# Kernel optimization log

Measured on AMD Instinct MI355X. Metric: run time of the kernel, lower is better.

The kernel has to match this reference:

```python
import jax, jax.numpy as jnp
import numpy as np
import math

D_MODEL = 1024
NHEAD = 16
D_HEAD = D_MODEL // NHEAD
TAU = 300.0
DELTA = 5.0 * 60.0  # delta_minutes -> seconds


def setup_inputs() -> dict:
    key = jax.random.key(0)
    ks = jax.random.split(key, 10)
    B, M = 4, 2048
    H = jax.random.normal(ks[0], (B, M, D_MODEL), dtype=jnp.float32)
    patch_mask = jax.random.randint(ks[1], (B, M), 0, 2).astype(jnp.int32)
    s = 1.0 / math.sqrt(D_MODEL)
    Wq = jax.random.normal(ks[2], (D_MODEL, D_MODEL), dtype=jnp.float32) * s
    bq = jnp.zeros((D_MODEL,), dtype=jnp.float32)
    Wk = jax.random.normal(ks[3], (D_MODEL, D_MODEL), dtype=jnp.float32) * s
    bk = jnp.zeros((D_MODEL,), dtype=jnp.float32)
    Wv = jax.random.normal(ks[4], (D_MODEL, D_MODEL), dtype=jnp.float32) * s
    bv = jnp.zeros((D_MODEL,), dtype=jnp.float32)
    Wo = jax.random.normal(ks[5], (D_MODEL, D_MODEL), dtype=jnp.float32) * s
    bo = jnp.zeros((D_MODEL,), dtype=jnp.float32)
    return {"H": H, "patch_mask": patch_mask, "Wq": Wq, "bq": bq,
            "Wk": Wk, "bk": bk, "Wv": Wv, "bv": bv, "Wo": Wo, "bo": bo}


def _time_bias(M):
    idx = jnp.arange(M)
    dist = jnp.abs(idx[:, None] - idx[None, :]).astype(jnp.float32) * DELTA
    w = jnp.exp(-dist / max(TAU, 1e-6))
    return jnp.log(w + 1e-12)  # (M, M)


def reference(H, patch_mask, Wq, bq, Wk, bk, Wv, bv, Wo, bo):
    B, M, D = H.shape
    nh, dh = NHEAD, D_HEAD
    # projections -> (B, nh, M, dh)
    q = (H @ Wq.T + bq).reshape(B, M, nh, dh).transpose(0, 2, 1, 3)
    k = (H @ Wk.T + bk).reshape(B, M, nh, dh).transpose(0, 2, 1, 3)
    v = (H @ Wv.T + bv).reshape(B, M, nh, dh).transpose(0, 2, 1, 3)
    attn = jnp.einsum('bhqd,bhkd->bhqk', q, k) / math.sqrt(dh)
    attn = attn + _time_bias(M)[None, None, :, :]
    key_pad = patch_mask <= 0  # (B, M)
    attn = jnp.where(key_pad[:, None, None, :], -1e9, attn)
    A = jax.nn.softmax(attn, axis=-1)
    out = jnp.einsum('bhqk,bhkd->bhqd', A, v)
    out = out.transpose(0, 2, 1, 3).reshape(B, M, D)
    out = out @ Wo.T + bo
    out = out * patch_mask[:, :, None].astype(out.dtype)
    return out
```

## Files before the change

### kernel.cpp

```cpp
#include <hip/hip_runtime.h>
#include <stdint.h>

typedef short short8 __attribute__((ext_vector_type(8)));
typedef float f32x4 __attribute__((ext_vector_type(4)));

#define B_    4
#define M_    2048
#define D_    1024
#define NH_   16
#define DH_   64
#define LOG2E 1.44269504f

__device__ __forceinline__ short f2bf(float f) {
  union { float f; uint32_t u; } v; v.f = f;
  uint32_t r = (v.u + 0x7fffu + ((v.u >> 16) & 1u)) >> 16;
  return (short)r;
}

__device__ __forceinline__ void gl_lds16(const void* g, void* l) {
  __builtin_amdgcn_global_load_lds(
      (__attribute__((address_space(1))) void*)(g),
      (__attribute__((address_space(3))) void*)(l),
      16, 0, 0);
}

__device__ __forceinline__ f32x4 mfma16(short8 a, short8 b, f32x4 c) {
  return __builtin_amdgcn_mfma_f32_16x16x32_bf16(a, b, c, 0, 0, 0);
}

__global__ __launch_bounds__(256) void cvt_all(const float* __restrict__ H,
                                               const float* __restrict__ s0,
                                               const float* __restrict__ s1,
                                               const float* __restrict__ s2,
                                               const float* __restrict__ s3,
                                               short* __restrict__ dH,
                                               short* __restrict__ d0,
                                               short* __restrict__ d1,
                                               short* __restrict__ d2,
                                               short* __restrict__ d3) {
  const int bidx = blockIdx.x;
  const float* src;
  short* dst;
  int i;
  if (bidx < 8192) {
    src = H; dst = dH; i = bidx * 256 + threadIdx.x;
  } else {
    const int y = (bidx - 8192) >> 10;
    src = (y == 0) ? s0 : (y == 1) ? s1 : (y == 2) ? s2 : s3;
    dst = (y == 0) ? d0 : (y == 1) ? d1 : (y == 2) ? d2 : d3;
    i = ((bidx - 8192) & 1023) * 256 + threadIdx.x;
  }
  float4 v = ((const float4*)src)[i];
  short4 o;
  o.x = f2bf(v.x); o.y = f2bf(v.y); o.z = f2bf(v.z); o.w = f2bf(v.w);
  ((short4*)dst)[i] = o;
}

__global__ __launch_bounds__(256, 3) void gemm_qkv(const short* __restrict__ A,
                                                   const short* __restrict__ Wqb,
                                                   const short* __restrict__ Wkb,
                                                   const short* __restrict__ Wvb,
                                                   const float* __restrict__ bq,
                                                   const float* __restrict__ bk,
                                                   const float* __restrict__ bv,
                                                   short* __restrict__ Qo,
                                                   short* __restrict__ Ko,
                                                   short* __restrict__ Vo) {
  __shared__ char smem_raw[34816];
  short* Ab0 = (short*)smem_raw;
  short* Ab1 = (short*)(smem_raw + 8192);
  short* Bb0 = (short*)(smem_raw + 16384);
  short* Bb1 = (short*)(smem_raw + 24576);

  const int L = blockIdx.x + 8 * (blockIdx.y + 64 * blockIdx.z);
  const int xcd = L & 7;
  const int s = L >> 3;
  const int m_local = s & 7;
  const int nz = s >> 3;
  const int nt = nz & 7, z = nz >> 3;
  const int m0 = (xcd * 8 + m_local) * 128;
  const int n0 = nt * 128;

  const short* Bt = (z == 0) ? Wqb : (z == 1) ? Wkb : Wvb;
  const float* bias = (z == 0) ? bq : (z == 1) ? bk : bv;
  const float scale = (z == 0) ? 0.125f : 1.0f;

  const int tid = threadIdx.x;
  const int w = tid >> 6, l = tid & 63;
  const int q4 = l >> 4, c = l & 15;
  const int wr = w >> 1, wc = w & 1;

  f32x4 acc[4][4] = {};
  const int arow = (l >> 2);
  const int acol = (l & 3) * 8;

#pragma unroll
  for (int st = 0; st < 2; ++st) {
    const int chunk = w * 2 + st;
    gl_lds16(A + (size_t)(m0 + chunk * 16 + arow) * 1024 + acol, Ab0 + chunk * 512);
    gl_lds16(Bt + (size_t)(n0 + chunk * 16 + arow) * 1024 + acol, Bb0 + chunk * 512);
  }
  __syncthreads();

  for (int kk = 0; kk < 32; ++kk) {
    const int cur = kk & 1;
    if (kk + 1 < 32) {
      const int k0n = (kk + 1) * 32;
#pragma unroll
      for (int st = 0; st < 2; ++st) {
        const int chunk = w * 2 + st;
        gl_lds16(A + (size_t)(m0 + chunk * 16 + arow) * 1024 + k0n + acol,
                 (cur ? Ab0 : Ab1) + chunk * 512);
        gl_lds16(Bt + (size_t)(n0 + chunk * 16 + arow) * 1024 + k0n + acol,
                 (cur ? Bb0 : Bb1) + chunk * 512);
      }
    }
    const short* Ab = cur ? Ab1 : Ab0;
    const short* Bb = cur ? Bb1 : Bb0;
    short8 af[4], bfr[4];
#pragma unroll
    for (int i = 0; i < 4; ++i)
      af[i] = *(const short8*)(Ab + (wr * 64 + i * 16 + c) * 32 + q4 * 8);
#pragma unroll
    for (int j = 0; j < 4; ++j)
      bfr[j] = *(const short8*)(Bb + (wc * 64 + j * 16 + c) * 32 + q4 * 8);
#pragma unroll
    for (int i = 0; i < 4; ++i)
#pragma unroll
      for (int j = 0; j < 4; ++j)
        acc[i][j] = mfma16(af[i], bfr[j], acc[i][j]);
    __syncthreads();
  }

  if (z < 2) {
    short* Cb = (short*)smem_raw;
    short* out = (z == 0) ? Qo : Ko;
#pragma unroll
    for (int j = 0; j < 4; ++j) {
      const float bvv = bias[n0 + wc * 64 + j * 16 + c];
#pragma unroll
      for (int i = 0; i < 4; ++i)
#pragma unroll
        for (int r = 0; r < 4; ++r)
          Cb[(wr * 64 + i * 16 + q4 * 4 + r) * 136 + wc * 64 + j * 16 + c] =
              f2bf((acc[i][j][r] + bvv) * scale);
    }
    __syncthreads();
#pragma unroll
    for (int p = 0; p < 8; ++p) {
      const int g = p * 256 + tid;
      const int row = g >> 4, seg = g & 15;
      *(short8*)(out + (size_t)(m0 + row) * 1024 + n0 + seg * 8) =
          *(const short8*)(Cb + row * 136 + seg * 8);
    }
  } else {
    short* Cb = (short*)smem_raw;
#pragma unroll
    for (int j = 0; j < 4; ++j) {
      const float bvv = bias[n0 + wc * 64 + j * 16 + c];
#pragma unroll
      for (int i = 0; i < 4; ++i) {
        short4 pk;
        pk.x = f2bf(acc[i][j][0] + bvv);
        pk.y = f2bf(acc[i][j][1] + bvv);
        pk.z = f2bf(acc[i][j][2] + bvv);
        pk.w = f2bf(acc[i][j][3] + bvv);
        *(short4*)(Cb + (wc * 64 + j * 16 + c) * 136 + wr * 64 + i * 16 + q4 * 4) = pk;
      }
    }
    __syncthreads();
    const int bb = m0 >> 11;
    const int tokb = m0 & 2047;
#pragma unroll
    for (int p = 0; p < 8; ++p) {
      const int g = p * 256 + tid;
      const int col = g >> 4, rseg = g & 15;
      const int colg = n0 + col;
      const int hh = colg >> 6, dd = colg & 63;
      *(short8*)(Vo + ((size_t)(bb * NH_ + hh) * DH_ + dd) * M_ + tokb + rseg * 8) =
          *(const short8*)(Cb + col * 136 + rseg * 8);
    }
  }
}

__global__ __launch_bounds__(256) void gemm_oproj(const short* __restrict__ A,
                                                  const short* __restrict__ Bt,
                                                  const float* __restrict__ bias,
                                                  const int* __restrict__ pmask,
                                                  float* __restrict__ outp) {
  __shared__ char smem[24576];
  short* Ab0 = (short*)smem;
  short* Ab1 = (short*)(smem + 8192);
  short* Bb0 = (short*)(smem + 16384);
  short* Bb1 = (short*)(smem + 20480);

  const int L = blockIdx.x + 16 * blockIdx.y;
  const int xcd = L & 7;
  const int s = L >> 3;
  const int m_local = s & 7;
  const int nt = s >> 3;
  const int m0 = (xcd * 8 + m_local) * 128;
  const int n0 = nt * 64;

  const int tid = threadIdx.x;
  const int w = tid >> 6, l = tid & 63;
  const int q4 = l >> 4, c = l & 15;
  const int wr = w >> 1, wc = w & 1;

  f32x4 acc[4][2] = {};
  const int arow = (l >> 2);
  const int acol = (l & 3) * 8;

#pragma unroll
  for (int st = 0; st < 2; ++st) {
    const int chunk = w * 2 + st;
    gl_lds16(A + (size_t)(m0 + chunk * 16 + arow) * 1024 + acol, Ab0 + chunk * 512);
  }
  gl_lds16(Bt + (size_t)(n0 + w * 16 + arow) * 1024 + acol, Bb0 + w * 512);
  __syncthreads();

  for (int kk = 0; kk < 32; ++kk) {
    const int cur = kk & 1;
    if (kk + 1 < 32) {
      const int k0n = (kk + 1) * 32;
#pragma unroll
      for (int st = 0; st < 2; ++st) {
        const int chunk = w * 2 + st;
        gl_lds16(A + (size_t)(m0 + chunk * 16 + arow) * 1024 + k0n + acol,
                 (cur ? Ab0 : Ab1) + chunk * 512);
      }
      gl_lds16(Bt + (size_t)(n0 + w * 16 + arow) * 1024 + k0n + acol,
               (cur ? Bb0 : Bb1) + w * 512);
    }
    const short* Ab = cur ? Ab1 : Ab0;
    const short* Bb = cur ? Bb1 : Bb0;
    short8 af[4], bfr[2];
#pragma unroll
    for (int i = 0; i < 4; ++i)
      af[i] = *(const short8*)(Ab + (wr * 64 + i * 16 + c) * 32 + q4 * 8);
#pragma unroll
    for (int j = 0; j < 2; ++j)
      bfr[j] = *(const short8*)(Bb + (wc * 32 + j * 16 + c) * 32 + q4 * 8);
#pragma unroll
    for (int i = 0; i < 4; ++i)
#pragma unroll
      for (int j = 0; j < 2; ++j)
        acc[i][j] = mfma16(af[i], bfr[j], acc[i][j]);
    __syncthreads();
  }

  float* Cf = (float*)smem;
#pragma unroll
  for (int half = 0; half < 2; ++half) {
    __syncthreads();
    if (wr == half) {
#pragma unroll
      for (int j = 0; j < 2; ++j) {
        const float bvv = bias[n0 + wc * 32 + j * 16 + c];
#pragma unroll
        for (int i = 0; i < 4; ++i)
#pragma unroll
          for (int r = 0; r < 4; ++r)
            Cf[(i * 16 + q4 * 4 + r) * 68 + wc * 32 + j * 16 + c] =
                acc[i][j][r] + bvv;
      }
    }
    __syncthreads();
#pragma unroll
    for (int p = 0; p < 4; ++p) {
      const int g = p * 256 + tid;
      const int row = g >> 4, seg = g & 15;
      const int rowg = m0 + half * 64 + row;
      const float mmv = (pmask[rowg] > 0) ? 1.0f : 0.0f;
      float4 v = *(const float4*)(Cf + row * 68 + seg * 4);
      v.x *= mmv; v.y *= mmv; v.z *= mmv; v.w *= mmv;
      *(float4*)(outp + (size_t)rowg * 1024 + n0 + seg * 4) = v;
    }
  }
}

__global__ __launch_bounds__(256) void attn_kernel(const short* __restrict__ Qb,
                                                   const short* __restrict__ Kb,
                                                   const short* __restrict__ Vtb,
                                                   const int* __restrict__ pmask,
                                                   short* __restrict__ Attb) {
  __shared__ char smem[20480];
  short* Ks0 = (short*)smem;
  short* Ks1 = (short*)(smem + 4096);
  short* Vs0 = (short*)(smem + 8192);
  short* Vs1 = (short*)(smem + 12288);
  short* Ps  = (short*)(smem + 16384);

  const int tid = threadIdx.x;
  const int w = tid >> 6, l = tid & 63;
  const int q4 = l >> 4, c = l & 15;
  const int qt = blockIdx.x, h = blockIdx.y, b = blockIdx.z;
  const short* Qrow = Qb + (size_t)(b * M_) * D_ + h * DH_;
  const short* Kbase = Kb + (size_t)(b * M_) * D_ + h * DH_;
  const short* Vbase = Vtb + (size_t)(b * NH_ + h) * DH_ * M_;
  const int qrow0 = qt * 64 + w * 16;

  short8 aq0 = *(const short8*)(Qrow + (size_t)(qrow0 + c) * D_ + q4 * 8);
  short8 aq1 = *(const short8*)(Qrow + (size_t)(qrow0 + c) * D_ + 32 + q4 * 8);

  const int jt0 = max(0, 2 * qt - 2);
  const int jt1 = min(M_ / 32 - 1, 2 * qt + 3);

  const int kh = tid >> 7, krow = (tid >> 2) & 31, ch = tid & 3;
  const int vrow = tid >> 2;

  {
    const int j0 = jt0 * 32;
    gl_lds16(Kbase + (size_t)(j0 + krow) * D_ + kh * 32 + ch * 8, (char*)Ks0 + tid * 16);
    gl_lds16(Vbase + (size_t)vrow * M_ + j0 + ch * 8, (char*)Vs0 + tid * 16);
  }
  __syncthreads();

  f32x4 o[4] = {};
  float lrun[4] = {0.f, 0.f, 0.f, 0.f};
  short* Pw = Ps + w * 512;

  for (int jt = jt0; jt <= jt1; ++jt) {
    const int buf = (jt - jt0) & 1;
    const int j0 = jt * 32;
    if (jt < jt1) {
      const int j0n = j0 + 32;
      gl_lds16(Kbase + (size_t)(j0n + krow) * D_ + kh * 32 + ch * 8,
               (char*)(buf ? Ks0 : Ks1) + tid * 16);
      gl_lds16(Vbase + (size_t)vrow * M_ + j0n + ch * 8,
               (char*)(buf ? Vs0 : Vs1) + tid * 16);
    }
    const short* Kt = buf ? Ks1 : Ks0;
    const short* Vt = buf ? Vs1 : Vs0;
    short8 b00 = *(const short8*)(Kt + c * 32 + q4 * 8);
    short8 b10 = *(const short8*)(Kt + 1024 + c * 32 + q4 * 8);
    short8 b01 = *(const short8*)(Kt + (16 + c) * 32 + q4 * 8);
    short8 b11 = *(const short8*)(Kt + 1024 + (16 + c) * 32 + q4 * 8);
    f32x4 s0 = {}, s1 = {};
    s0 = mfma16(aq0, b00, s0);
    s0 = mfma16(aq1, b10, s0);
    s1 = mfma16(aq0, b01, s1);
    s1 = mfma16(aq1, b11, s1);

    const float w0m = (pmask[b * M_ + j0 + c] > 0) ? 1.f : 0.f;
    const float w1m = (pmask[b * M_ + j0 + 16 + c] > 0) ? 1.f : 0.f;

#pragma unroll
    for (int r = 0; r < 4; ++r) {
      const int qr = qrow0 + q4 * 4 + r;
      const float d0 = fminf(fabsf((float)(qr - (j0 + c))), 28.0f);
      const float d1 = fminf(fabsf((float)(qr - (j0 + 16 + c))), 28.0f);
      const float p0 = exp2f((s0[r] - d0) * LOG2E) * w0m;
      const float p1 = exp2f((s1[r] - d1) * LOG2E) * w1m;
      Pw[(q4 * 4 + r) * 32 + c] = f2bf(p0);
      Pw[(q4 * 4 + r) * 32 + 16 + c] = f2bf(p1);
      lrun[r] += p0 + p1;
    }
    short8 pa = *(const short8*)(Pw + c * 32 + q4 * 8);
#pragma unroll
    for (int f = 0; f < 4; ++f) {
      short8 bv = *(const short8*)(Vt + (f * 16 + c) * 32 + q4 * 8);
      o[f] = mfma16(pa, bv, o[f]);
    }
    __syncthreads();
  }

#pragma unroll
  for (int r = 0; r < 4; ++r) {
#pragma unroll
    for (int off = 1; off < 16; off <<= 1)
      lrun[r] += __shfl_xor(lrun[r], off);
  }

  short* Cb = (short*)smem;
#pragma unroll
  for (int r = 0; r < 4; ++r) {
    const float inv = 1.0f / lrun[r];
#pragma unroll
    for (int f = 0; f < 4; ++f)
      Cb[(w * 16 + q4 * 4 + r) * 72 + f * 16 + c] = f2bf(o[f][r] * inv);
  }
  __syncthreads();
#pragma unroll
  for (int p = 0; p < 2; ++p) {
    const int u = p * 256 + tid;
    const int row = u >> 3, seg = u & 7;
    *(short8*)(Attb + (size_t)(b * M_ + qt * 64 + row) * D_ + h * DH_ + seg * 8) =
        *(const short8*)(Cb + row * 72 + seg * 8);
  }
}

extern "C" void kernel_launch(void* const* d_in, const int* in_sizes, int n_in,
                              void* d_out, int out_size, void* d_ws, size_t ws_size,
                              hipStream_t stream) {
  const float* H     = (const float*)d_in[0];
  const int*   pmask = (const int*)d_in[1];
  const float* Wq    = (const float*)d_in[2];
  const float* bq    = (const float*)d_in[3];
  const float* Wk    = (const float*)d_in[4];
  const float* bk    = (const float*)d_in[5];
  const float* Wv    = (const float*)d_in[6];
  const float* bv    = (const float*)d_in[7];
  const float* Wo    = (const float*)d_in[8];
  const float* bo    = (const float*)d_in[9];
  float* out = (float*)d_out;
  char* ws = (char*)d_ws;

  short* Hb   = (short*)(ws);
  short* Attb = (short*)(ws);
  short* Wqb  = (short*)(ws + (16u << 20));
  short* Wkb  = (short*)(ws + (18u << 20));
  short* Wvb  = (short*)(ws + (20u << 20));
  short* Wob  = (short*)(ws + (22u << 20));
  short* Qb   = (short*)(ws + (24u << 20));
  short* Kb2  = (short*)(ws + (40u << 20));
  short* Vtb  = (short*)(ws + (56u << 20));

  cvt_all<<<8192 + 4096, 256, 0, stream>>>(H, Wq, Wk, Wv, Wo,
                                           Hb, Wqb, Wkb, Wvb, Wob);

  dim3 gq(8, 64, 3);
  gemm_qkv<<<gq, 256, 0, stream>>>(Hb, Wqb, Wkb, Wvb, bq, bk, bv, Qb, Kb2, Vtb);

  attn_kernel<<<dim3(M_ / 64, NH_, B_), 256, 0, stream>>>(Qb, Kb2, Vtb, pmask, Attb);

  gemm_oproj<<<dim3(16, 64), 256, 0, stream>>>(Attb, Wob, bo, pmask, out);
}
```

Baseline: 231.7 us.

## Fuse Q/K/V projections into one GEMM block sharing the A tile, add LDS swizzle

Each block now computes all three Q, K and V output tiles, loading the H tile once and reusing it across three weight tiles, so grid z shrinks from 3 to 1. LDS grows to 64KB and accumulators triple, so launch bounds drop to 2 blocks per CU and the block count falls to 512. An XOR swizzle on the LDS column layout is also added to reduce bank conflicts on the fragment reads. The cost is lower occupancy, higher register pressure and fewer blocks to fill the GPU.

```diff
diff --git a/kernel.cpp b/kernel.cpp
--- a/kernel.cpp
+++ b/kernel.cpp
@@ -56,7 +56,7 @@
   ((short4*)dst)[i] = o;
 }
 
-__global__ __launch_bounds__(256, 3) void gemm_qkv(const short* __restrict__ A,
+__global__ __launch_bounds__(256, 2) void gemm_qkv(const short* __restrict__ A,
                                                    const short* __restrict__ Wqb,
                                                    const short* __restrict__ Wkb,
                                                    const short* __restrict__ Wvb,
@@ -66,39 +66,40 @@
                                                    short* __restrict__ Qo,
                                                    short* __restrict__ Ko,
                                                    short* __restrict__ Vo) {
-  __shared__ char smem_raw[34816];
+  __shared__ char smem_raw[65536];
   short* Ab0 = (short*)smem_raw;
   short* Ab1 = (short*)(smem_raw + 8192);
-  short* Bb0 = (short*)(smem_raw + 16384);
-  short* Bb1 = (short*)(smem_raw + 24576);
-
-  const int L = blockIdx.x + 8 * (blockIdx.y + 64 * blockIdx.z);
+
+  const int L = blockIdx.x + 8 * blockIdx.y;
   const int xcd = L & 7;
   const int s = L >> 3;
   const int m_local = s & 7;
-  const int nz = s >> 3;
-  const int nt = nz & 7, z = nz >> 3;
+  const int nt = s >> 3;
   const int m0 = (xcd * 8 + m_local) * 128;
   const int n0 = nt * 128;
-
-  const short* Bt = (z == 0) ? Wqb : (z == 1) ? Wkb : Wvb;
-  const float* bias = (z == 0) ? bq : (z == 1) ? bk : bv;
-  const float scale = (z == 0) ? 0.125f : 1.0f;
 
   const int tid = threadIdx.x;
   const int w = tid >> 6, l = tid & 63;
   const int q4 = l >> 4, c = l & 15;
   const int wr = w >> 1, wc = w & 1;
 
-  f32x4 acc[4][4] = {};
+  f32x4 acc[3][4][4] = {};
   const int arow = (l >> 2);
-  const int acol = (l & 3) * 8;
+  const int acol = ((l & 3) ^ ((l >> 3) & 3)) * 8;
+  const int q4s = (q4 ^ ((c >> 1) & 3)) * 8;
+
+  const short* Bz0 = Wqb;
+  const short* Bz1 = Wkb;
+  const short* Bz2 = Wvb;
 
 #pragma unroll
   for (int st = 0; st < 2; ++st) {
     const int chunk = w * 2 + st;
-    gl_lds16(A + (size_t)(m0 + chunk * 16 + arow) * 1024 + acol, Ab0 + chunk * 512);
-    gl_lds16(Bt + (size_t)(n0 + chunk * 16 + arow) * 1024 + acol, Bb0 + chunk * 512);
+    const size_t roff = (size_t)(chunk * 16 + arow) * 1024 + acol;
+    gl_lds16(A + (size_t)m0 * 1024 + roff, Ab0 + chunk * 512);
+    gl_lds16(Bz0 + (size_t)n0 * 1024 + roff, (short*)(smem_raw + 16384) + chunk * 512);
+    gl_lds16(Bz1 + (size_t)n0 * 1024 + roff, (short*)(smem_raw + 32768) + chunk * 512);
+    gl_lds16(Bz2 + (size_t)n0 * 1024 + roff, (short*)(smem_raw + 49152) + chunk * 512);
   }
   __syncthreads();
 
@@ -109,32 +110,44 @@
 #pragma unroll
       for (int st = 0; st < 2; ++st) {
         const int chunk = w * 2 + st;
-        gl_lds16(A + (size_t)(m0 + chunk * 16 + arow) * 1024 + k0n + acol,
-                 (cur ? Ab0 : Ab1) + chunk * 512);
-        gl_lds16(Bt + (size_t)(n0 + chunk * 16 + arow) * 1024 + k0n + acol,
-                 (cur ? Bb0 : Bb1) + chunk * 512);
+        const size_t roff = (size_t)(chunk * 16 + arow) * 1024 + k0n + acol;
+        gl_lds16(A + (size_t)m0 * 1024 + roff, (cur ? Ab0 : Ab1) + chunk * 512);
+        gl_lds16(Bz0 + (size_t)n0 * 1024 + roff,
+                 (short*)(smem_raw + 16384 + (cur ? 0 : 8192)) + chunk * 512);
+        gl_lds16(Bz1 + (size_t)n0 * 1024 + roff,
+                 (short*)(smem_raw + 32768 + (cur ? 0 : 8192)) + chunk * 512);
+        gl_lds16(Bz2 + (size_t)n0 * 1024 + roff,
+                 (short*)(smem_raw + 49152 + (cur ? 0 : 8192)) + chunk * 512);
       }
     }
     const short* Ab = cur ? Ab1 : Ab0;
-    const short* Bb = cur ? Bb1 : Bb0;
-    short8 af[4], bfr[4];
+    short8 af[4];
 #pragma unroll
     for (int i = 0; i < 4; ++i)
-      af[i] = *(const short8*)(Ab + (wr * 64 + i * 16 + c) * 32 + q4 * 8);
-#pragma unroll
-    for (int j = 0; j < 4; ++j)
-      bfr[j] = *(const short8*)(Bb + (wc * 64 + j * 16 + c) * 32 + q4 * 8);
-#pragma unroll
-    for (int i = 0; i < 4; ++i)
+      af[i] = *(const short8*)(Ab + (wr * 64 + i * 16 + c) * 32 + q4s);
+#pragma unroll
+    for (int z = 0; z < 3; ++z) {
+      const short* Bb =
+          (const short*)(smem_raw + 16384 + z * 16384 + (cur ? 8192 : 0));
+      short8 bfr[4];
 #pragma unroll
       for (int j = 0; j < 4; ++j)
-        acc[i][j] = mfma16(af[i], bfr[j], acc[i][j]);
-    __syncthreads();
-  }
-
-  if (z < 2) {
+        bfr[j] = *(const short8*)(Bb + (wc * 64 + j * 16 + c) * 32 + q4s);
+#pragma unroll
+      for (int i = 0; i < 4; ++i)
+#pragma unroll
+        for (int j = 0; j < 4; ++j)
+          acc[z][i][j] = mfma16(af[i], bfr[j], acc[z][i][j]);
+    }
+    __syncthreads();
+  }
+
+#pragma unroll
+  for (int z = 0; z < 2; ++z) {
     short* Cb = (short*)smem_raw;
-    short* out = (z == 0) ? Qo : Ko;
+    const float* bias = z ? bk : bq;
+    short* outp = z ? Ko : Qo;
+    const float scale = z ? 1.0f : 0.125f;
 #pragma unroll
     for (int j = 0; j < 4; ++j) {
       const float bvv = bias[n0 + wc * 64 + j * 16 + c];
@@ -143,28 +156,30 @@
 #pragma unroll
         for (int r = 0; r < 4; ++r)
           Cb[(wr * 64 + i * 16 + q4 * 4 + r) * 136 + wc * 64 + j * 16 + c] =
-              f2bf((acc[i][j][r] + bvv) * scale);
+              f2bf((acc[z][i][j][r] + bvv) * scale);
     }
     __syncthreads();
 #pragma unroll
     for (int p = 0; p < 8; ++p) {
       const int g = p * 256 + tid;
       const int row = g >> 4, seg = g & 15;
-      *(short8*)(out + (size_t)(m0 + row) * 1024 + n0 + seg * 8) =
+      *(short8*)(outp + (size_t)(m0 + row) * 1024 + n0 + seg * 8) =
           *(const short8*)(Cb + row * 136 + seg * 8);
     }
-  } else {
+    __syncthreads();
+  }
+  {
     short* Cb = (short*)smem_raw;
 #pragma unroll
     for (int j = 0; j < 4; ++j) {
-      const float bvv = bias[n0 + wc * 64 + j * 16 + c];
+      const float bvv = bv[n0 + wc * 64 + j * 16 + c];
 #pragma unroll
       for (int i = 0; i < 4; ++i) {
         short4 pk;
-        pk.x = f2bf(acc[i][j][0] + bvv);
-        pk.y = f2bf(acc[i][j][1] + bvv);
-        pk.z = f2bf(acc[i][j][2] + bvv);
-        pk.w = f2bf(acc[i][j][3] + bvv);
+        pk.x = f2bf(acc[2][i][j][0] + bvv);
+        pk.y = f2bf(acc[2][i][j][1] + bvv);
+        pk.z = f2bf(acc[2][i][j][2] + bvv);
+        pk.w = f2bf(acc[2][i][j][3] + bvv);
         *(short4*)(Cb + (wc * 64 + j * 16 + c) * 136 + wr * 64 + i * 16 + q4 * 4) = pk;
       }
     }
@@ -419,8 +434,8 @@
   cvt_all<<<8192 + 4096, 256, 0, stream>>>(H, Wq, Wk, Wv, Wo,
                                            Hb, Wqb, Wkb, Wvb, Wob);
 
-  dim3 gq(8, 64, 3);
-  gemm_qkv<<<gq, 256, 0, stream>>>(Hb, Wqb, Wkb, Wvb, bq, bk, bv, Qb, Kb2, Vtb);
+  gemm_qkv<<<dim3(8, 64), 256, 0, stream>>>(Hb, Wqb, Wkb, Wvb, bq, bk, bv,
+                                            Qb, Kb2, Vtb);
 
   attn_kernel<<<dim3(M_ / 64, NH_, B_), 256, 0, stream>>>(Qb, Kb2, Vtb, pmask, Attb);
 
```

After: 213.0 us. 1.09x faster.
